# Performance work log

Measured on AMD Instinct MI355X. Metric: run time of the kernel, lower is better.

Reference implementation:

```python
import jax, jax.numpy as jnp
import numpy as np

B, HOR, L, A, HID = 4096, 32, 512, 64, 1024


def _linear_params(key, fan_in, fan_out):
    kw, kb = jax.random.split(key)
    bound = 1.0 / np.sqrt(fan_in)
    W = jax.random.uniform(kw, (fan_in, fan_out), jnp.float32, -bound, bound)
    b = jax.random.uniform(kb, (fan_out,), jnp.float32, -bound, bound)
    return W, b


def setup_inputs() -> dict:
    key = jax.random.key(0)
    ks = jax.random.split(key, 11)
    initial_state = jax.random.normal(ks[0], (B, L), jnp.float32)
    action_sequence = jax.random.normal(ks[1], (B, HOR, A), jnp.float32)
    Wae, bae = _linear_params(ks[2], A, A)
    Wt1, bt1 = _linear_params(ks[3], L + A, HID)
    Wt2, bt2 = _linear_params(ks[4], HID, HID)
    Wt3, bt3 = _linear_params(ks[5], HID, L)
    Wo1, bo1 = _linear_params(ks[6], L, HID)
    Wo2, bo2 = _linear_params(ks[7], HID, L)
    Wh1, bh1 = _linear_params(ks[8], L + A, HID)
    Wh2, bh2 = _linear_params(ks[9], HID, 1)
    return dict(initial_state=initial_state, action_sequence=action_sequence,
                Wae=Wae, bae=bae, Wt1=Wt1, bt1=bt1, Wt2=Wt2, bt2=bt2,
                Wt3=Wt3, bt3=bt3, Wo1=Wo1, bo1=bo1, Wo2=Wo2, bo2=bo2,
                Wh1=Wh1, bh1=bh1, Wh2=Wh2, bh2=bh2)


def reference(initial_state, action_sequence, Wae, bae, Wt1, bt1, Wt2, bt2,
              Wt3, bt3, Wo1, bo1, Wo2, bo2, Wh1, bh1, Wh2, bh2):
    # rollout: sequential scan over horizon steps
    def step(state, action):
        # harm predictor on raw (state, action)
        sa = jnp.concatenate([state, action], axis=-1)            # [B, L+A]
        harm = jax.nn.sigmoid(jax.nn.relu(sa @ Wh1 + bh1) @ Wh2 + bh2)  # [B,1]
        # observation predictor on current state
        obs = jax.nn.relu(state @ Wo1 + bo1) @ Wo2 + bo2          # [B, L]
        # transition on (state, encoded action); residual update
        ae = action @ Wae + bae                                   # [B, A]
        sae = jnp.concatenate([state, ae], axis=-1)               # [B, L+A]
        h = jax.nn.relu(sae @ Wt1 + bt1)
        h = jax.nn.relu(h @ Wt2 + bt2)
        next_state = state + h @ Wt3 + bt3                        # [B, L]
        return next_state, (next_state, obs, harm[:, 0])

    actions_t = jnp.swapaxes(action_sequence, 0, 1)               # [HOR, B, A]
    _, (states_t, obs_t, harm_t) = jax.lax.scan(step, initial_state, actions_t)
    # states: initial + all next states -> [B, HOR+1, L]
    states = jnp.concatenate([initial_state[:, None, :],
                              jnp.swapaxes(states_t, 0, 1)], axis=1)
    observations = jnp.swapaxes(obs_t, 0, 1)                      # [B, HOR, L]
    harm_predictions = jnp.swapaxes(harm_t, 0, 1)                 # [B, HOR]
    return states, observations, harm_predictions
```

## Files before the change

### kernel.cpp

```cpp
#include <hip/hip_runtime.h>
#include <math.h>

#define B_ 4096
#define HOR_ 32
#define L_ 512
#define A_ 64
#define HID_ 1024

#define CB 512
#define MC (CB * HOR_)

typedef unsigned short ushort_t;
typedef __attribute__((ext_vector_type(4))) float f32x4;
typedef __attribute__((ext_vector_type(8))) short s16x8;
typedef __attribute__((ext_vector_type(4))) short s16x4;
typedef __attribute__((ext_vector_type(8))) _Float16 f16x8;

__device__ __forceinline__ unsigned short bf16_rne(float x) {
    unsigned u = __builtin_bit_cast(unsigned, x);
    u += 0x7fffu + ((u >> 16) & 1u);
    return (unsigned short)(u >> 16);
}
__device__ __forceinline__ float bf16_to_f32(unsigned short h) {
    unsigned u = ((unsigned)h) << 16;
    return __builtin_bit_cast(float, u);
}

template <int BMT, bool TWOSRC, bool SPLIT_OUT, bool RELU, bool RESID, bool F32OUT>
__global__ __launch_bounds__(512, 4) void trans_gemm(
    const _Float16* __restrict__ Ahi, const _Float16* __restrict__ Alo,
    int lda, int K,
    const float* __restrict__ Aae, int lda_ae, int aoff,
    const _Float16* __restrict__ Whi, const _Float16* __restrict__ Wlo,
    const float* __restrict__ bias,
    const float* __restrict__ resid, int ldr,
    _Float16* __restrict__ Ohi, _Float16* __restrict__ Olo, int ldoh,
    float* __restrict__ Of, int ldof)
{
    __shared__ _Float16 Ah[2][BMT][40];
    __shared__ _Float16 Al[2][BMT][40];
    __shared__ _Float16 Bh[2][128][40];
    __shared__ _Float16 Bl[2][128][40];

    const int tid = threadIdx.x;
    const int m0 = blockIdx.y * BMT;
    const int n0 = blockIdx.x * 128;
    const int w = tid >> 6, l = tid & 63;
    const int wm = w >> 2, wn = w & 3;
    const int kg = l >> 4, lr = l & 15;
    constexpr int AF = BMT / 32;

    const int srow = tid >> 2, sg = tid & 3;
    const bool doA = (BMT == 128) || (tid < 256);

    f32x4 acc[AF][2] = {};
    f16x8 rAh, rAl, rBh, rBl;

    const _Float16* pBh = Whi + (size_t)(n0 + srow) * K + sg * 8;
    const _Float16* pBl = Wlo + (size_t)(n0 + srow) * K + sg * 8;
    const _Float16* pAh = Ahi + (size_t)(m0 + (doA ? srow : 0)) * lda + sg * 8;
    const _Float16* pAl = Alo + (size_t)(m0 + (doA ? srow : 0)) * lda + sg * 8;
    const float* pAe = TWOSRC
        ? (Aae + (size_t)(m0 + (doA ? srow : 0)) * lda_ae + aoff + sg * 8)
        : nullptr;

    auto load_regs = [&](int ks) {
        const int k0 = ks * 32;
        rBh = *reinterpret_cast<const f16x8*>(pBh + k0);
        rBl = *reinterpret_cast<const f16x8*>(pBl + k0);
        if (doA) {
            if (!TWOSRC || k0 < L_) {
                rAh = *reinterpret_cast<const f16x8*>(pAh + k0);
                rAl = *reinterpret_cast<const f16x8*>(pAl + k0);
            } else {
                const float* s = pAe + (k0 - L_);
                float4 v0 = *reinterpret_cast<const float4*>(s);
                float4 v1 = *reinterpret_cast<const float4*>(s + 4);
                float vv[8] = {v0.x, v0.y, v0.z, v0.w, v1.x, v1.y, v1.z, v1.w};
                f16x8 h, lo;
#pragma unroll
                for (int j = 0; j < 8; ++j) {
                    _Float16 hh = (_Float16)vv[j];
                    h[j] = hh;
                    lo[j] = (_Float16)(vv[j] - (float)hh);
                }
                rAh = h; rAl = lo;
            }
        }
    };
    auto write_lds = [&](int buf) {
        *reinterpret_cast<f16x8*>(&Bh[buf][srow][sg * 8]) = rBh;
        *reinterpret_cast<f16x8*>(&Bl[buf][srow][sg * 8]) = rBl;
        if (doA) {
            *reinterpret_cast<f16x8*>(&Ah[buf][srow][sg * 8]) = rAh;
            *reinterpret_cast<f16x8*>(&Al[buf][srow][sg * 8]) = rAl;
        }
    };

    const int NT = K / 32;
    load_regs(0);
    write_lds(0);
    __syncthreads();
    int cur = 0;

    for (int ks = 0; ks < NT; ++ks) {
        if (ks + 1 < NT) load_regs(ks + 1);

        f16x8 ah[AF], al[AF], bh[2], bl[2];
#pragma unroll
        for (int i = 0; i < AF; ++i) {
            int r = wm * (BMT / 2) + i * 16 + lr;
            ah[i] = *reinterpret_cast<const f16x8*>(&Ah[cur][r][kg * 8]);
            al[i] = *reinterpret_cast<const f16x8*>(&Al[cur][r][kg * 8]);
        }
#pragma unroll
        for (int j = 0; j < 2; ++j) {
            int r = wn * 32 + j * 16 + lr;
            bh[j] = *reinterpret_cast<const f16x8*>(&Bh[cur][r][kg * 8]);
            bl[j] = *reinterpret_cast<const f16x8*>(&Bl[cur][r][kg * 8]);
        }
#pragma unroll
        for (int i = 0; i < AF; ++i)
#pragma unroll
            for (int j = 0; j < 2; ++j) {
                acc[i][j] = __builtin_amdgcn_mfma_f32_16x16x32_f16(
                    ah[i], bh[j], acc[i][j], 0, 0, 0);
                acc[i][j] = __builtin_amdgcn_mfma_f32_16x16x32_f16(
                    ah[i], bl[j], acc[i][j], 0, 0, 0);
                acc[i][j] = __builtin_amdgcn_mfma_f32_16x16x32_f16(
                    al[i], bh[j], acc[i][j], 0, 0, 0);
            }

        if (ks + 1 < NT) {
            write_lds(cur ^ 1);
            __syncthreads();
            cur ^= 1;
        }
    }

    float bv[2];
#pragma unroll
    for (int j = 0; j < 2; ++j) bv[j] = bias[n0 + wn * 32 + j * 16 + lr];

#pragma unroll
    for (int i = 0; i < AF; ++i)
#pragma unroll
        for (int j = 0; j < 2; ++j)
#pragma unroll
            for (int r = 0; r < 4; ++r) {
                int row = m0 + wm * (BMT / 2) + i * 16 + kg * 4 + r;
                int col = n0 + wn * 32 + j * 16 + lr;
                float v = acc[i][j][r] + bv[j];
                if (RESID)
                    v += resid[(size_t)row * ldr + col];
                if (RELU) v = fmaxf(v, 0.f);
                if (F32OUT)
                    Of[(size_t)row * ldof + col] = v;
                if (SPLIT_OUT) {
                    _Float16 h = (_Float16)v;
                    Ohi[(size_t)row * ldoh + col] = h;
                    Olo[(size_t)row * ldoh + col] = (_Float16)(v - (float)h);
                }
            }
}

__global__ __launch_bounds__(256) void split_transpose(
    const float* __restrict__ W, _Float16* __restrict__ Whi,
    _Float16* __restrict__ Wlo, int K, int N)
{
    int k = blockIdx.x * 256 + threadIdx.x;
    int n = blockIdx.y;
    if (k < K) {
        float v = W[(size_t)k * N + n];
        _Float16 h = (_Float16)v;
        Whi[(size_t)n * K + k] = h;
        Wlo[(size_t)n * K + k] = (_Float16)(v - (float)h);
    }
}

__global__ __launch_bounds__(256) void ae_all(
    const float* __restrict__ actions,
    const float* __restrict__ Wae,
    const float* __restrict__ bae,
    float* __restrict__ ae)
{
    const long r = (long)blockIdx.x * 4 + (threadIdx.x >> 6);
    const int c = threadIdx.x & 63;
    const float* arow = actions + r * 64;
    float acc = bae[c];
#pragma unroll 16
    for (int k = 0; k < 64; ++k) acc = fmaf(arow[k], Wae[k * 64 + c], acc);
    ae[r * 64 + c] = acc;
}

__global__ __launch_bounds__(256) void ae_step(
    const float* __restrict__ actions, const float* __restrict__ Wae,
    const float* __restrict__ bae, int t, float* __restrict__ aeS)
{
    const long b = (long)blockIdx.x * 4 + (threadIdx.x >> 6);
    const int c = threadIdx.x & 63;
    const float* arow = actions + (b * HOR_ + t) * 64;
    float acc = bae[c];
#pragma unroll 16
    for (int k = 0; k < 64; ++k) acc = fmaf(arow[k], Wae[k * 64 + c], acc);
    aeS[b * 64 + c] = acc;
}

__global__ __launch_bounds__(256) void init_split(
    const float* __restrict__ init, float* __restrict__ states,
    _Float16* __restrict__ sth, _Float16* __restrict__ stl)
{
    size_t i = (size_t)blockIdx.x * 256 + threadIdx.x;
    size_t b = i >> 9, l = i & 511;
    float v = init[i];
    states[b * (33 * L_) + l] = v;
    _Float16 h = (_Float16)v;
    sth[i] = h;
    stl[i] = (_Float16)(v - (float)h);
}


__global__ __launch_bounds__(256) void cast_transpose(
    const float* __restrict__ W, ushort_t* __restrict__ WT, int K, int N)
{
    int k = blockIdx.x * 256 + threadIdx.x;
    int n = blockIdx.y;
    if (k < K) WT[(long)n * K + k] = bf16_rne(W[(long)k * N + n]);
}

__global__ __launch_bounds__(256) void mm_split(
    const float* __restrict__ Astate,
    const float* __restrict__ Aact,
    int Ktot,
    const ushort_t* __restrict__ WT,
    int N,
    const float* __restrict__ bias,
    ushort_t* __restrict__ Out)
{
    __shared__ ushort_t Ahi[128][40];
    __shared__ ushort_t Alo[128][40];
    __shared__ ushort_t Bt[128][40];

    const int tid = threadIdx.x;
    const int m0 = blockIdx.y * 128;
    const int n0 = blockIdx.x * 128;
    const int w = tid >> 6;
    const int l = tid & 63;
    const int wm = w >> 1, wn = w & 1;
    const int kg = l >> 4, lr = l & 15;

    f32x4 acc[4][4] = {};

    for (int k0 = 0; k0 < Ktot; k0 += 32) {
#pragma unroll
        for (int s = 0; s < 4; ++s) {
            int idx = tid + s * 256;
            int arow = idx >> 3;
            int ch = idx & 7;
            int m = m0 + arow;
            const float* src;
            if (k0 < L_) {
                src = Astate + (long)((m >> 5) * 33 + (m & 31)) * L_ + k0 + ch * 4;
            } else {
                src = Aact + (long)m * A_ + (k0 - L_) + ch * 4;
            }
            float4 v = *reinterpret_cast<const float4*>(src);
            unsigned short h0 = bf16_rne(v.x), h1 = bf16_rne(v.y),
                           h2 = bf16_rne(v.z), h3 = bf16_rne(v.w);
            unsigned short e0 = bf16_rne(v.x - bf16_to_f32(h0));
            unsigned short e1 = bf16_rne(v.y - bf16_to_f32(h1));
            unsigned short e2 = bf16_rne(v.z - bf16_to_f32(h2));
            unsigned short e3 = bf16_rne(v.w - bf16_to_f32(h3));
            s16x4 hv = {(short)h0, (short)h1, (short)h2, (short)h3};
            s16x4 lv = {(short)e0, (short)e1, (short)e2, (short)e3};
            *reinterpret_cast<s16x4*>(&Ahi[arow][ch * 4]) = hv;
            *reinterpret_cast<s16x4*>(&Alo[arow][ch * 4]) = lv;
        }
#pragma unroll
        for (int s = 0; s < 2; ++s) {
            int idx = tid + s * 256;
            int brow = idx >> 2;
            int ch = idx & 3;
            s16x8 wv = *reinterpret_cast<const s16x8*>(
                &WT[(long)(n0 + brow) * Ktot + k0 + ch * 8]);
            *reinterpret_cast<s16x8*>(&Bt[brow][ch * 8]) = wv;
        }
        __syncthreads();

        s16x8 ah[4], al[4], bb[4];
#pragma unroll
        for (int i = 0; i < 4; ++i) {
            int r = wm * 64 + i * 16 + lr;
            ah[i] = *reinterpret_cast<const s16x8*>(&Ahi[r][kg * 8]);
            al[i] = *reinterpret_cast<const s16x8*>(&Alo[r][kg * 8]);
        }
#pragma unroll
        for (int j = 0; j < 4; ++j) {
            int r = wn * 64 + j * 16 + lr;
            bb[j] = *reinterpret_cast<const s16x8*>(&Bt[r][kg * 8]);
        }
#pragma unroll
        for (int i = 0; i < 4; ++i)
#pragma unroll
            for (int j = 0; j < 4; ++j) {
                acc[i][j] = __builtin_amdgcn_mfma_f32_16x16x32_bf16(
                    ah[i], bb[j], acc[i][j], 0, 0, 0);
                acc[i][j] = __builtin_amdgcn_mfma_f32_16x16x32_bf16(
                    al[i], bb[j], acc[i][j], 0, 0, 0);
            }
        __syncthreads();
    }

    float bv[4];
#pragma unroll
    for (int j = 0; j < 4; ++j) bv[j] = bias[n0 + wn * 64 + j * 16 + lr];
#pragma unroll
    for (int i = 0; i < 4; ++i)
#pragma unroll
        for (int j = 0; j < 4; ++j)
#pragma unroll
            for (int r = 0; r < 4; ++r) {
                int row = m0 + wm * 64 + i * 16 + kg * 4 + r;
                int col = n0 + wn * 64 + j * 16 + lr;
                float v = fmaxf(acc[i][j][r] + bv[j], 0.f);
                Out[(long)row * N + col] = bf16_rne(v);
            }
}

__global__ __launch_bounds__(256) void mm_bf16(
    const ushort_t* __restrict__ Abf,
    const ushort_t* __restrict__ WT,
    int N,
    const float* __restrict__ bias,
    float* __restrict__ Out)
{
    __shared__ ushort_t At[128][40];
    __shared__ ushort_t Bt[128][40];

    const int tid = threadIdx.x;
    const int m0 = blockIdx.y * 128;
    const int n0 = blockIdx.x * 128;
    const int w = tid >> 6;
    const int l = tid & 63;
    const int wm = w >> 1, wn = w & 1;
    const int kg = l >> 4, lr = l & 15;

    f32x4 acc[4][4] = {};

    for (int k0 = 0; k0 < HID_; k0 += 32) {
#pragma unroll
        for (int s = 0; s < 2; ++s) {
            int idx = tid + s * 256;
            int arow = idx >> 2;
            int ch = idx & 3;
            s16x8 av = *reinterpret_cast<const s16x8*>(
                &Abf[(long)(m0 + arow) * HID_ + k0 + ch * 8]);
            *reinterpret_cast<s16x8*>(&At[arow][ch * 8]) = av;
        }
#pragma unroll
        for (int s = 0; s < 2; ++s) {
            int idx = tid + s * 256;
            int brow = idx >> 2;
            int ch = idx & 3;
            s16x8 wv = *reinterpret_cast<const s16x8*>(
                &WT[(long)(n0 + brow) * HID_ + k0 + ch * 8]);
            *reinterpret_cast<s16x8*>(&Bt[brow][ch * 8]) = wv;
        }
        __syncthreads();

        s16x8 aa[4], bb[4];
#pragma unroll
        for (int i = 0; i < 4; ++i)
            aa[i] = *reinterpret_cast<const s16x8*>(&At[wm * 64 + i * 16 + lr][kg * 8]);
#pragma unroll
        for (int j = 0; j < 4; ++j)
            bb[j] = *reinterpret_cast<const s16x8*>(&Bt[wn * 64 + j * 16 + lr][kg * 8]);
#pragma unroll
        for (int i = 0; i < 4; ++i)
#pragma unroll
            for (int j = 0; j < 4; ++j)
                acc[i][j] = __builtin_amdgcn_mfma_f32_16x16x32_bf16(
                    aa[i], bb[j], acc[i][j], 0, 0, 0);
        __syncthreads();
    }

    float bv[4];
#pragma unroll
    for (int j = 0; j < 4; ++j) bv[j] = bias[n0 + wn * 64 + j * 16 + lr];
#pragma unroll
    for (int i = 0; i < 4; ++i)
#pragma unroll
        for (int j = 0; j < 4; ++j)
#pragma unroll
            for (int r = 0; r < 4; ++r) {
                int row = m0 + wm * 64 + i * 16 + kg * 4 + r;
                int col = n0 + wn * 64 + j * 16 + lr;
                Out[(long)row * N + col] = acc[i][j][r] + bv[j];
            }
}

__global__ __launch_bounds__(256) void harm_reduce(
    const ushort_t* __restrict__ hh,
    const float* __restrict__ Wh2,
    const float* __restrict__ bh2,
    float* __restrict__ harm)
{
    const int wave = threadIdx.x >> 6;
    const int lane = threadIdx.x & 63;
    const long r = (long)blockIdx.x * 4 + wave;
    const ushort_t* row = hh + r * HID_;
    float s = 0.f;
#pragma unroll
    for (int q = 0; q < 2; ++q) {
        s16x8 a = *reinterpret_cast<const s16x8*>(&row[lane * 16 + q * 8]);
        float4 w0 = *reinterpret_cast<const float4*>(&Wh2[lane * 16 + q * 8]);
        float4 w1 = *reinterpret_cast<const float4*>(&Wh2[lane * 16 + q * 8 + 4]);
        s = fmaf(bf16_to_f32((unsigned short)a[0]), w0.x, s);
        s = fmaf(bf16_to_f32((unsigned short)a[1]), w0.y, s);
        s = fmaf(bf16_to_f32((unsigned short)a[2]), w0.z, s);
        s = fmaf(bf16_to_f32((unsigned short)a[3]), w0.w, s);
        s = fmaf(bf16_to_f32((unsigned short)a[4]), w1.x, s);
        s = fmaf(bf16_to_f32((unsigned short)a[5]), w1.y, s);
        s = fmaf(bf16_to_f32((unsigned short)a[6]), w1.z, s);
        s = fmaf(bf16_to_f32((unsigned short)a[7]), w1.w, s);
    }
#pragma unroll
    for (int off = 32; off; off >>= 1) s += __shfl_down(s, off);
    if (lane == 0) {
        float x = s + bh2[0];
        harm[r] = 1.f / (1.f + expf(-x));
    }
}

extern "C" void kernel_launch(void* const* d_in, const int* in_sizes, int n_in,
                              void* d_out, int out_size, void* d_ws, size_t ws_size,
                              hipStream_t stream)
{
    const float* initial = (const float*)d_in[0];
    const float* actions = (const float*)d_in[1];
    const float* Wae = (const float*)d_in[2];
    const float* bae = (const float*)d_in[3];
    const float* Wt1 = (const float*)d_in[4];
    const float* bt1 = (const float*)d_in[5];
    const float* Wt2 = (const float*)d_in[6];
    const float* bt2 = (const float*)d_in[7];
    const float* Wt3 = (const float*)d_in[8];
    const float* bt3 = (const float*)d_in[9];
    const float* Wo1 = (const float*)d_in[10];
    const float* bo1 = (const float*)d_in[11];
    const float* Wo2 = (const float*)d_in[12];
    const float* bo2 = (const float*)d_in[13];
    const float* Wh1 = (const float*)d_in[14];
    const float* bh1 = (const float*)d_in[15];
    const float* Wh2 = (const float*)d_in[16];
    const float* bh2 = (const float*)d_in[17];

    float* out = (float*)d_out;
    float* states = out;
    float* obs = out + (size_t)B_ * 33 * L_;
    float* harm = obs + (size_t)B_ * HOR_ * L_;

    char* wsb = (char*)d_ws;
    size_t off = 0;
    auto alloc = [&](size_t bytes) { char* q = wsb + off; off += bytes; return q; };
    ushort_t* WT_o1 = (ushort_t*)alloc((size_t)HID_ * L_ * 2);
    ushort_t* WT_o2 = (ushort_t*)alloc((size_t)L_ * HID_ * 2);
    ushort_t* WT_h1 = (ushort_t*)alloc((size_t)HID_ * 576 * 2);
    _Float16* Wt1h = (_Float16*)alloc((size_t)HID_ * 576 * 2);
    _Float16* Wt1l = (_Float16*)alloc((size_t)HID_ * 576 * 2);
    _Float16* Wt2h = (_Float16*)alloc((size_t)HID_ * HID_ * 2);
    _Float16* Wt2l = (_Float16*)alloc((size_t)HID_ * HID_ * 2);
    _Float16* Wt3h = (_Float16*)alloc((size_t)L_ * HID_ * 2);
    _Float16* Wt3l = (_Float16*)alloc((size_t)L_ * HID_ * 2);
    _Float16* sth  = (_Float16*)alloc((size_t)B_ * L_ * 2);
    _Float16* stl  = (_Float16*)alloc((size_t)B_ * L_ * 2);
    _Float16* h1h  = (_Float16*)alloc((size_t)B_ * HID_ * 2);
    _Float16* h1l  = (_Float16*)alloc((size_t)B_ * HID_ * 2);
    _Float16* h2h  = (_Float16*)alloc((size_t)B_ * HID_ * 2);
    _Float16* h2l  = (_Float16*)alloc((size_t)B_ * HID_ * 2);
    float* ae = (float*)alloc(0);
    const size_t need_batched = off + (size_t)B_ * HOR_ * A_ * 4;
    const bool batched_ae = (ws_size >= need_batched);

    ushort_t* oh = (ushort_t*)h1h;

    cast_transpose<<<dim3(2, HID_), 256, 0, stream>>>(Wo1, WT_o1, L_, HID_);
    cast_transpose<<<dim3(4, L_), 256, 0, stream>>>(Wo2, WT_o2, HID_, L_);
    cast_transpose<<<dim3(3, HID_), 256, 0, stream>>>(Wh1, WT_h1, 576, HID_);
    split_transpose<<<dim3(3, HID_), 256, 0, stream>>>(Wt1, Wt1h, Wt1l, 576, HID_);
    split_transpose<<<dim3(4, HID_), 256, 0, stream>>>(Wt2, Wt2h, Wt2l, HID_, HID_);
    split_transpose<<<dim3(4, L_), 256, 0, stream>>>(Wt3, Wt3h, Wt3l, HID_, L_);

    init_split<<<(B_ * L_) / 256, 256, 0, stream>>>(initial, states, sth, stl);
    if (batched_ae)
        ae_all<<<(B_ * HOR_) / 4, 256, 0, stream>>>(actions, Wae, bae, ae);

    const int ldS = 33 * L_;
    const int lda_ae = batched_ae ? (HOR_ * A_) : A_;

    for (int t = 0; t < HOR_; ++t) {
        if (!batched_ae)
            ae_step<<<B_ / 4, 256, 0, stream>>>(actions, Wae, bae, t, ae);
        const int aoff = batched_ae ? t * A_ : 0;
        trans_gemm<128, true, true, true, false, false>
            <<<dim3(HID_ / 128, B_ / 128), 512, 0, stream>>>(
            sth, stl, L_, 576, ae, lda_ae, aoff,
            Wt1h, Wt1l, bt1, nullptr, 0, h1h, h1l, HID_, nullptr, 0);
        trans_gemm<128, false, true, true, false, false>
            <<<dim3(HID_ / 128, B_ / 128), 512, 0, stream>>>(
            h1h, h1l, HID_, HID_, nullptr, 0, 0,
            Wt2h, Wt2l, bt2, nullptr, 0, h2h, h2l, HID_, nullptr, 0);
        trans_gemm<64, false, true, false, true, true>
            <<<dim3(L_ / 128, B_ / 64), 512, 0, stream>>>(
            h2h, h2l, HID_, HID_, nullptr, 0, 0,
            Wt3h, Wt3l, bt3, states + (size_t)t * L_, ldS,
            sth, stl, L_, states + (size_t)(t + 1) * L_, ldS);
    }

    for (int c = 0; c < B_ / CB; ++c) {
        const float* Sc = states + (size_t)c * CB * 33 * L_;
        const float* Ac = actions + (size_t)c * CB * HOR_ * A_;
        mm_split<<<dim3(HID_ / 128, MC / 128), 256, 0, stream>>>(
            Sc, nullptr, L_, WT_o1, HID_, bo1, oh);
        mm_bf16<<<dim3(L_ / 128, MC / 128), 256, 0, stream>>>(
            oh, WT_o2, L_, bo2, obs + (size_t)c * CB * HOR_ * L_);
        mm_split<<<dim3(HID_ / 128, MC / 128), 256, 0, stream>>>(
            Sc, Ac, 576, WT_h1, HID_, bh1, oh);
        harm_reduce<<<MC / 4, 256, 0, stream>>>(
            oh, Wh2, bh2, harm + (size_t)c * CB * HOR_);
    }
}
```

Baseline: 4.428 ms.

## Load weight fragments directly into registers and swizzle block order in transition GEMM

The transition GEMM stops staging the weight (B) tiles through shared memory. Each wave now loads its hi/lo weight fragments straight from global memory into registers, double-buffered across K steps, while only the activation tile goes through LDS. The warp layout becomes 4x2 waves over 128 rows and BF*32 columns. Blocks are remapped in groups of eight for L2 locality, the third GEMM moves to 128x64 tiles, and launch bounds drop to 2 blocks per CU. This removes the LDS traffic and bank pressure for B, at the cost of more registers, lower occupancy, and uncoalesced 16-byte global loads of the weights.

```diff
diff --git a/kernel.cpp b/kernel.cpp
--- a/kernel.cpp
+++ b/kernel.cpp
@@ -26,8 +26,8 @@
     return __builtin_bit_cast(float, u);
 }
 
-template <int BMT, bool TWOSRC, bool SPLIT_OUT, bool RELU, bool RESID, bool F32OUT>
-__global__ __launch_bounds__(512, 4) void trans_gemm(
+template <int BF, bool TWOSRC, bool SPLIT_OUT, bool RELU, bool RESID, bool F32OUT>
+__global__ __launch_bounds__(512, 2) void trans_gemm(
     const _Float16* __restrict__ Ahi, const _Float16* __restrict__ Alo,
     int lda, int K,
     const float* __restrict__ Aae, int lda_ae, int aoff,
@@ -37,92 +37,95 @@
     _Float16* __restrict__ Ohi, _Float16* __restrict__ Olo, int ldoh,
     float* __restrict__ Of, int ldof)
 {
-    __shared__ _Float16 Ah[2][BMT][40];
-    __shared__ _Float16 Al[2][BMT][40];
-    __shared__ _Float16 Bh[2][128][40];
-    __shared__ _Float16 Bl[2][128][40];
+    __shared__ _Float16 Ah[2][128][40];
+    __shared__ _Float16 Al[2][128][40];
+
+    const int gx = gridDim.x;
+    const int nwg = gx * gridDim.y;
+    int bid = blockIdx.y * gx + blockIdx.x;
+    const int cpx = nwg >> 3;
+    bid = (bid & 7) * cpx + (bid >> 3);
+    const int m0 = (bid / gx) * 128;
+    const int n0 = (bid % gx) * (BF * 32);
 
     const int tid = threadIdx.x;
-    const int m0 = blockIdx.y * BMT;
-    const int n0 = blockIdx.x * 128;
     const int w = tid >> 6, l = tid & 63;
-    const int wm = w >> 2, wn = w & 3;
+    const int wr = w >> 1, wc = w & 1;
     const int kg = l >> 4, lr = l & 15;
-    constexpr int AF = BMT / 32;
 
     const int srow = tid >> 2, sg = tid & 3;
-    const bool doA = (BMT == 128) || (tid < 256);
-
-    f32x4 acc[AF][2] = {};
-    f16x8 rAh, rAl, rBh, rBl;
-
-    const _Float16* pBh = Whi + (size_t)(n0 + srow) * K + sg * 8;
-    const _Float16* pBl = Wlo + (size_t)(n0 + srow) * K + sg * 8;
-    const _Float16* pAh = Ahi + (size_t)(m0 + (doA ? srow : 0)) * lda + sg * 8;
-    const _Float16* pAl = Alo + (size_t)(m0 + (doA ? srow : 0)) * lda + sg * 8;
+
+    f32x4 acc[2][BF] = {};
+    f16x8 rAh, rAl;
+    f16x8 bh[BF], bl[BF], bhn[BF], bln[BF];
+
+    const size_t brow = (size_t)(n0 + wc * (BF * 16) + lr) * K + kg * 8;
+    const _Float16* pWh = Whi + brow;
+    const _Float16* pWl = Wlo + brow;
+
+    const _Float16* pAh = Ahi + (size_t)(m0 + srow) * lda + sg * 8;
+    const _Float16* pAl = Alo + (size_t)(m0 + srow) * lda + sg * 8;
     const float* pAe = TWOSRC
-        ? (Aae + (size_t)(m0 + (doA ? srow : 0)) * lda_ae + aoff + sg * 8)
+        ? (Aae + (size_t)(m0 + srow) * lda_ae + aoff + sg * 8)
         : nullptr;
 
-    auto load_regs = [&](int ks) {
+    auto load_A_regs = [&](int ks) {
         const int k0 = ks * 32;
-        rBh = *reinterpret_cast<const f16x8*>(pBh + k0);
-        rBl = *reinterpret_cast<const f16x8*>(pBl + k0);
-        if (doA) {
-            if (!TWOSRC || k0 < L_) {
-                rAh = *reinterpret_cast<const f16x8*>(pAh + k0);
-                rAl = *reinterpret_cast<const f16x8*>(pAl + k0);
-            } else {
-                const float* s = pAe + (k0 - L_);
-                float4 v0 = *reinterpret_cast<const float4*>(s);
-                float4 v1 = *reinterpret_cast<const float4*>(s + 4);
-                float vv[8] = {v0.x, v0.y, v0.z, v0.w, v1.x, v1.y, v1.z, v1.w};
-                f16x8 h, lo;
-#pragma unroll
-                for (int j = 0; j < 8; ++j) {
-                    _Float16 hh = (_Float16)vv[j];
-                    h[j] = hh;
-                    lo[j] = (_Float16)(vv[j] - (float)hh);
-                }
-                rAh = h; rAl = lo;
-            }
+        if (!TWOSRC || k0 < L_) {
+            rAh = *reinterpret_cast<const f16x8*>(pAh + k0);
+            rAl = *reinterpret_cast<const f16x8*>(pAl + k0);
+        } else {
+            const float* s = pAe + (k0 - L_);
+            float4 v0 = *reinterpret_cast<const float4*>(s);
+            float4 v1 = *reinterpret_cast<const float4*>(s + 4);
+            float vv[8] = {v0.x, v0.y, v0.z, v0.w, v1.x, v1.y, v1.z, v1.w};
+            f16x8 h, lo;
+#pragma unroll
+            for (int j = 0; j < 8; ++j) {
+                _Float16 hh = (_Float16)vv[j];
+                h[j] = hh;
+                lo[j] = (_Float16)(vv[j] - (float)hh);
+            }
+            rAh = h; rAl = lo;
         }
     };
-    auto write_lds = [&](int buf) {
-        *reinterpret_cast<f16x8*>(&Bh[buf][srow][sg * 8]) = rBh;
-        *reinterpret_cast<f16x8*>(&Bl[buf][srow][sg * 8]) = rBl;
-        if (doA) {
-            *reinterpret_cast<f16x8*>(&Ah[buf][srow][sg * 8]) = rAh;
-            *reinterpret_cast<f16x8*>(&Al[buf][srow][sg * 8]) = rAl;
-        }
+    auto write_A_lds = [&](int buf) {
+        *reinterpret_cast<f16x8*>(&Ah[buf][srow][sg * 8]) = rAh;
+        *reinterpret_cast<f16x8*>(&Al[buf][srow][sg * 8]) = rAl;
     };
+    auto load_B = [&](int ks, f16x8* h, f16x8* lo) {
+        const int k0 = ks * 32;
+#pragma unroll
+        for (int j = 0; j < BF; ++j) {
+            h[j]  = *reinterpret_cast<const f16x8*>(pWh + (size_t)j * 16 * K + k0);
+            lo[j] = *reinterpret_cast<const f16x8*>(pWl + (size_t)j * 16 * K + k0);
+        }
+    };
 
     const int NT = K / 32;
-    load_regs(0);
-    write_lds(0);
+    load_A_regs(0);
+    load_B(0, bh, bl);
+    write_A_lds(0);
     __syncthreads();
     int cur = 0;
 
     for (int ks = 0; ks < NT; ++ks) {
-        if (ks + 1 < NT) load_regs(ks + 1);
-
-        f16x8 ah[AF], al[AF], bh[2], bl[2];
-#pragma unroll
-        for (int i = 0; i < AF; ++i) {
-            int r = wm * (BMT / 2) + i * 16 + lr;
+        if (ks + 1 < NT) {
+            load_A_regs(ks + 1);
+            load_B(ks + 1, bhn, bln);
+        }
+
+        f16x8 ah[2], al[2];
+#pragma unroll
+        for (int i = 0; i < 2; ++i) {
+            int r = wr * 32 + i * 16 + lr;
             ah[i] = *reinterpret_cast<const f16x8*>(&Ah[cur][r][kg * 8]);
             al[i] = *reinterpret_cast<const f16x8*>(&Al[cur][r][kg * 8]);
         }
 #pragma unroll
-        for (int j = 0; j < 2; ++j) {
-            int r = wn * 32 + j * 16 + lr;
-            bh[j] = *reinterpret_cast<const f16x8*>(&Bh[cur][r][kg * 8]);
-            bl[j] = *reinterpret_cast<const f16x8*>(&Bl[cur][r][kg * 8]);
-        }
-#pragma unroll
-        for (int i = 0; i < AF; ++i)
-#pragma unroll
-            for (int j = 0; j < 2; ++j) {
+        for (int i = 0; i < 2; ++i)
+#pragma unroll
+            for (int j = 0; j < BF; ++j) {
                 acc[i][j] = __builtin_amdgcn_mfma_f32_16x16x32_f16(
                     ah[i], bh[j], acc[i][j], 0, 0, 0);
                 acc[i][j] = __builtin_amdgcn_mfma_f32_16x16x32_f16(
@@ -132,24 +135,27 @@
             }
 
         if (ks + 1 < NT) {
-            write_lds(cur ^ 1);
+            write_A_lds(cur ^ 1);
             __syncthreads();
             cur ^= 1;
-        }
-    }
-
-    float bv[2];
-#pragma unroll
-    for (int j = 0; j < 2; ++j) bv[j] = bias[n0 + wn * 32 + j * 16 + lr];
-
-#pragma unroll
-    for (int i = 0; i < AF; ++i)
-#pragma unroll
-        for (int j = 0; j < 2; ++j)
+#pragma unroll
+            for (int j = 0; j < BF; ++j) { bh[j] = bhn[j]; bl[j] = bln[j]; }
+        }
+    }
+
+    float bv[BF];
+#pragma unroll
+    for (int j = 0; j < BF; ++j)
+        bv[j] = bias[n0 + wc * (BF * 16) + j * 16 + lr];
+
+#pragma unroll
+    for (int i = 0; i < 2; ++i)
+#pragma unroll
+        for (int j = 0; j < BF; ++j)
 #pragma unroll
             for (int r = 0; r < 4; ++r) {
-                int row = m0 + wm * (BMT / 2) + i * 16 + kg * 4 + r;
-                int col = n0 + wn * 32 + j * 16 + lr;
+                int row = m0 + wr * 32 + i * 16 + kg * 4 + r;
+                int col = n0 + wc * (BF * 16) + j * 16 + lr;
                 float v = acc[i][j][r] + bv[j];
                 if (RESID)
                     v += resid[(size_t)row * ldr + col];
@@ -502,16 +508,16 @@
         if (!batched_ae)
             ae_step<<<B_ / 4, 256, 0, stream>>>(actions, Wae, bae, t, ae);
         const int aoff = batched_ae ? t * A_ : 0;
-        trans_gemm<128, true, true, true, false, false>
+        trans_gemm<4, true, true, true, false, false>
             <<<dim3(HID_ / 128, B_ / 128), 512, 0, stream>>>(
             sth, stl, L_, 576, ae, lda_ae, aoff,
             Wt1h, Wt1l, bt1, nullptr, 0, h1h, h1l, HID_, nullptr, 0);
-        trans_gemm<128, false, true, true, false, false>
+        trans_gemm<4, false, true, true, false, false>
             <<<dim3(HID_ / 128, B_ / 128), 512, 0, stream>>>(
             h1h, h1l, HID_, HID_, nullptr, 0, 0,
             Wt2h, Wt2l, bt2, nullptr, 0, h2h, h2l, HID_, nullptr, 0);
-        trans_gemm<64, false, true, false, true, true>
-            <<<dim3(L_ / 128, B_ / 64), 512, 0, stream>>>(
+        trans_gemm<2, false, true, false, true, true>
+            <<<dim3(L_ / 64, B_ / 128), 512, 0, stream>>>(
             h2h, h2l, HID_, HID_, nullptr, 0, 0,
             Wt3h, Wt3l, bt3, states + (size_t)t * L_, ldS,
             sth, stl, L_, states + (size_t)(t + 1) * L_, ldS);
```

New measurement: 7.322 ms. 1.65x slower.
